# Optimization experiments

Measured on AMD Instinct MI355X. Metric: run time of the kernel, lower is better.

Reference implementation:

```python
import jax, jax.numpy as jnp
import numpy as np

NUM_CLASSES = 80
STRIDES = (32, 16, 8)
SCORE_THRESH = 0.01
NMS_THRESH = 0.45
TOP_K = 200
PRE_K = 4096          # pre-NMS candidate cap (greedy NMS only ever emits TOP_K boxes)
NEG = -1e9            # 'suppressed' score sentinel (avoids -inf NaN issues)
CLS_OFFSET = 4096.0   # class-aware NMS: offset boxes per class (boxes live in [0, 608])

_ANCHORS_PX = [[(116, 90), (156, 198), (373, 326)],
               [(30, 61), (62, 45), (59, 119)],
               [(10, 13), (16, 30), (33, 23)]]


def setup_inputs() -> dict:
    key = jax.random.key(0)
    bs, img = 8, 608
    inp = {}
    for lvl, (stride, anc) in enumerate(zip(STRIDES, _ANCHORS_PX)):
        H = W = img // stride
        key, k = jax.random.split(key)
        inp[f"in{lvl}"] = jax.random.normal(k, (bs, 3 * (NUM_CLASSES + 5), H, W), dtype=jnp.float32)
        aw = jnp.array([a[0] / stride for a in anc], jnp.float32)
        ah = jnp.array([a[1] / stride for a in anc], jnp.float32)
        inp[f"aw{lvl}"] = jnp.broadcast_to(aw[None, :, None, None], (bs, 3, H, W))
        inp[f"ah{lvl}"] = jnp.broadcast_to(ah[None, :, None, None], (bs, 3, H, W))
        inp[f"gx{lvl}"] = jnp.broadcast_to(jnp.arange(W, dtype=jnp.float32)[None, None, None, :], (bs, 3, H, W))
        inp[f"gy{lvl}"] = jnp.broadcast_to(jnp.arange(H, dtype=jnp.float32)[None, None, :, None], (bs, 3, H, W))
    return inp


def _decode_level(x, aw, ah, gx, gy, stride):
    bs, _, H, W = x.shape
    x = x.reshape(bs, -1, NUM_CLASSES + 5, H, W).transpose(0, 1, 3, 4, 2)  # [bs,3,H,W,85]
    px = jax.nn.sigmoid(x[..., 0]) + gx
    py = jax.nn.sigmoid(x[..., 1]) + gy
    pw = jnp.exp(x[..., 2]) * aw
    ph = jnp.exp(x[..., 3]) * ah
    conf = jax.nn.sigmoid(x[..., 4])
    cls = jax.nn.sigmoid(x[..., 5:])
    boxes = jnp.stack([px, py, pw, ph], -1) * jnp.float32(stride)  # [bs,3,H,W,4] (cx,cy,w,h)
    return boxes.reshape(bs, -1, 4), conf.reshape(bs, -1), cls.reshape(bs, -1, NUM_CLASSES)


def _center_to_corner(b):
    cx, cy, w, h = b[..., 0], b[..., 1], b[..., 2], b[..., 3]
    return jnp.stack([cx - w / 2, cy - h / 2, cx + w / 2, cy + h / 2], -1)


def _nms_image(boxes, conf, cls):
    # boxes [N,4] corner, conf [N], cls [N,C]
    N, C = cls.shape
    scores = (conf[:, None] * cls).reshape(-1)                          # [N*C]
    cboxes = jnp.broadcast_to(boxes[:, None, :], (N, C, 4)).reshape(-1, 4)
    labels = jnp.broadcast_to(jnp.arange(C), (N, C)).reshape(-1)
    s = jnp.where(scores > SCORE_THRESH, scores, NEG)
    top_s, idx = jax.lax.top_k(s, PRE_K)
    b = cboxes[idx]                                                     # [PRE_K,4]
    l = labels[idx]
    ob = b + (l.astype(jnp.float32) * CLS_OFFSET)[:, None]              # class-aware offset
    area = (ob[:, 2] - ob[:, 0]) * (ob[:, 3] - ob[:, 1])

    def step(live, _):
        i = jnp.argmax(live)
        si, bi, ai = live[i], ob[i], area[i]
        x1 = jnp.maximum(bi[0], ob[:, 0]); y1 = jnp.maximum(bi[1], ob[:, 1])
        x2 = jnp.minimum(bi[2], ob[:, 2]); y2 = jnp.minimum(bi[3], ob[:, 3])
        inter = jnp.clip(x2 - x1, 0.0) * jnp.clip(y2 - y1, 0.0)
        iou = inter / (ai + area - inter + 1e-9)
        live = jnp.where(iou > NMS_THRESH, NEG, live)                   # suppresses self too
        return live, (i, si)

    _, (sel, sel_s) = jax.lax.scan(step, top_s, None, length=TOP_K)
    valid = sel_s > SCORE_THRESH
    out_b = jnp.where(valid[:, None], b[sel], 0.0)
    out_l = jnp.where(valid, l[sel], 0).astype(jnp.float32)
    out_s = jnp.where(valid, sel_s, 0.0)
    return jnp.concatenate([out_b, out_l[:, None], out_s[:, None]], -1)  # [TOP_K, 6]


def _forward(levels):
    boxes, conf, cls = [], [], []
    for (x, aw, ah, gx, gy), stride in zip(levels, STRIDES):
        bb, cc, cl = _decode_level(x, aw, ah, gx, gy, stride)
        boxes.append(bb); conf.append(cc); cls.append(cl)
    boxes = _center_to_corner(jnp.concatenate(boxes, 1))   # [bs,N,4]
    conf = jnp.concatenate(conf, 1)                        # [bs,N]
    cls = jnp.concatenate(cls, 1)                          # [bs,N,C]
    return jax.vmap(_nms_image)(boxes, conf, cls)          # [bs,TOP_K,6]


def reference(in0, aw0, ah0, gx0, gy0, in1, aw1, ah1, gx1, gy1, in2, aw2, ah2, gx2, gy2):
    levels = [(in0, aw0, ah0, gx0, gy0), (in1, aw1, ah1, gx1, gy1), (in2, aw2, ah2, gx2, gy2)]
    return _forward(levels)
```

## Files before the change

kernel.cpp:

```cpp
#include <hip/hip_runtime.h>
#include <stdint.h>

typedef unsigned int u32;
typedef unsigned long long u64;

#define NCLS 80
#define NBOX 22743
#define PREK 4096
#define BCAP 65536
#define NIMG 8
#define SCORE_TH 0.01f
#define IOU_TH 0.45f
#define TOPK 200

#define DCH 20
#define DNCH 4
#define GCH 10
#define GNCH 8

#define LCAP 1536

#define BKCAP 8
#define HCAP 224
#define HUGE_TH 3488.0f

#define RJC 4
#define RJW 1024

#define HIST_OFF 0
#define META_OFF 131072
#define CNT_OFF  131200
#define ZERO_BYTES 133248
#define WIN_OFF  133248
#define BND_OFF  395392
#define PART_OFF BND_OFF
#define BOX_OFF  4589696
#define SKEY_OFF 7500800
#define SOBOX_OFF 7762944
#define SAREA_OFF 8287232

__device__ __forceinline__ float sigmf(float x) { return 1.0f / (1.0f + expf(-x)); }

#define BIN_BASE 61440u

__device__ __forceinline__ u64 pad_key(int i) { return (u64)(~(u32)i); }

__global__ __launch_bounds__(256) void decode_hist_all(const float* __restrict__ in0,
                              const float* __restrict__ in1, const float* __restrict__ in2,
                              float4* __restrict__ boxes, u32* __restrict__ hist) {
  __shared__ u32 lh[4096];
  const int img = blockIdx.y;
  const int c0 = blockIdx.z * DCH;
  for (int i = threadIdx.x; i < 4096; i += 256) lh[i] = 0;
  __syncthreads();

  const int bx = blockIdx.x;
  if (bx < 5) {
    const int W = 19, HW = 361;
    const int r = bx * 256 + threadIdx.x;
    if (r < 3 * HW) {
      const int a = r / HW, p = r - a * HW;
      const int y = p / W, x = p - y * W;
      const float* base = in0 + ((size_t)(img * 255 + a * 85)) * (size_t)HW + p;
      float l[DCH];
#pragma unroll
      for (int k = 0; k < DCH; ++k) l[k] = base[(size_t)(5 + c0 + k) * HW];
      const float x4 = base[4 * (size_t)HW];
      if (c0 == 0) {
        const float aw = (a == 0) ? 3.625f : ((a == 1) ? 4.875f : 11.65625f);
        const float ah = (a == 0) ? 2.8125f : ((a == 1) ? 6.1875f : 10.1875f);
        const float x0 = base[0];
        const float x1 = base[(size_t)HW];
        const float x2 = base[2 * (size_t)HW];
        const float x3 = base[3 * (size_t)HW];
        const float px = sigmf(x0) + (float)x;
        const float py = sigmf(x1) + (float)y;
        const float pw = expf(x2) * aw;
        const float ph = expf(x3) * ah;
        const float cx = px * 32.f, cy = py * 32.f, bw = pw * 32.f, bh = ph * 32.f;
        boxes[(size_t)img * NBOX + r] =
            make_float4(cx - bw * 0.5f, cy - bh * 0.5f, cx + bw * 0.5f, cy + bh * 0.5f);
      }
      const float conf = sigmf(x4);
      if (conf > SCORE_TH) {
#pragma unroll
        for (int k = 0; k < DCH; ++k) {
          float s = conf * sigmf(l[k]);
          if (s > SCORE_TH) {
            u32 bin = (__float_as_uint(s) >> 14) - BIN_BASE;
            atomicAdd(&lh[bin], 1u);
          }
        }
      }
    }
  } else {
    const bool L1 = bx < 10;
    const float* in = L1 ? in1 : in2;
    const int W = L1 ? 38 : 76;
    const int HW = L1 ? 1444 : 5776;
    const int lvl_off = L1 ? 1083 : 5415;
    const float stride = L1 ? 16.f : 8.f;
    const int HW4 = HW >> 2;
    const int idx = (bx - (L1 ? 5 : 10)) * 256 + threadIdx.x;
    if (idx < 3 * HW4) {
      const int a = idx / HW4;
      const int p0 = (idx - a * HW4) << 2;
      const float* base = in + ((size_t)(img * 255 + a * 85)) * (size_t)HW + p0;
      float4 scv[DCH];
#pragma unroll
      for (int k = 0; k < DCH; ++k)
        scv[k] = *(const float4*)(base + (size_t)(5 + c0 + k) * HW);
      float4 v4 = *(const float4*)(base + 4 * (size_t)HW);
      const float* t4 = (const float*)&v4;
      float conf[4];
      if (c0 == 0) {
        const float aw = L1 ? ((a == 0) ? 1.875f : ((a == 1) ? 3.875f : 3.6875f))
                            : ((a == 0) ? 1.25f : ((a == 1) ? 2.f : 4.125f));
        const float ah = L1 ? ((a == 0) ? 3.8125f : ((a == 1) ? 2.8125f : 7.4375f))
                            : ((a == 0) ? 1.625f : ((a == 1) ? 3.75f : 2.875f));
        float4 v0 = *(const float4*)(base);
        float4 v1 = *(const float4*)(base + (size_t)HW);
        float4 v2 = *(const float4*)(base + 2 * (size_t)HW);
        float4 v3 = *(const float4*)(base + 3 * (size_t)HW);
        const float* t0 = (const float*)&v0;
        const float* t1 = (const float*)&v1;
        const float* t2 = (const float*)&v2;
        const float* t3 = (const float*)&v3;
        float4* bout = boxes + (size_t)img * NBOX + lvl_off + a * HW + p0;
#pragma unroll
        for (int i = 0; i < 4; ++i) {
          const int p = p0 + i;
          const int y = p / W, x = p - y * W;
          const float px = sigmf(t0[i]) + (float)x;
          const float py = sigmf(t1[i]) + (float)y;
          const float pw = expf(t2[i]) * aw;
          const float ph = expf(t3[i]) * ah;
          const float cx = px * stride, cy = py * stride, bw = pw * stride, bh = ph * stride;
          bout[i] = make_float4(cx - bw * 0.5f, cy - bh * 0.5f, cx + bw * 0.5f, cy + bh * 0.5f);
        }
      }
#pragma unroll
      for (int i = 0; i < 4; ++i) conf[i] = sigmf(t4[i]);
#pragma unroll
      for (int k = 0; k < DCH; ++k) {
        const float* s4 = (const float*)&scv[k];
#pragma unroll
        for (int i = 0; i < 4; ++i) {
          float s = conf[i] * sigmf(s4[i]);
          if (s > SCORE_TH) {
            u32 bin = (__float_as_uint(s) >> 14) - BIN_BASE;
            atomicAdd(&lh[bin], 1u);
          }
        }
      }
    }
  }
  __syncthreads();
  u32* gh = hist + (size_t)img * 4096;
  for (int i = threadIdx.x; i < 4096; i += 256) {
    u32 v = lh[i];
    if (v) atomicAdd(&gh[i], v);
  }
}

__global__ void scan_k(const u32* __restrict__ hist, int* __restrict__ meta) {
  const int img = blockIdx.x;
  const u32* h = hist + (size_t)img * 4096;
  __shared__ u32 lsum[256];
  __shared__ u32 above[256];
  __shared__ u32 s_total;
  const int t = threadIdx.x;
  u32 s = 0;
  for (int j = 0; j < 16; ++j) s += h[t * 16 + j];
  lsum[t] = s;
  __syncthreads();
  if (t == 0) {
    u32 acc = 0;
    for (int i = 255; i >= 0; --i) { above[i] = acc; acc += lsum[i]; }
    s_total = acc;
  }
  __syncthreads();
  const u32 K = PREK;
  int* m = meta + img * 4;
  if (s_total < K) {
    if (t == 0) { m[0] = -1; m[1] = 0; }
  } else {
    if (above[t] < K && above[t] + lsum[t] >= K) {
      u32 cum = above[t];
      for (int j = 15; j >= 0; --j) {
        u32 hv = h[t * 16 + j];
        cum += hv;
        if (cum >= K) { m[0] = t * 16 + j; m[1] = (int)(K - (cum - hv)); break; }
      }
    }
  }
}

__device__ __forceinline__ void flush_list(const u64* llist, int lcnt, int cap,
                                           int* gctr, u64* glist, int gcap) {
  __shared__ int gbase_s;
  int n = lcnt < cap ? lcnt : cap;
  if (threadIdx.x == 0) gbase_s = n ? atomicAdd(gctr, n) : 0;
  __syncthreads();
  const int gb = gbase_s;
  for (int i = threadIdx.x; i < n; i += 256) {
    int pos = gb + i;
    if (pos < gcap) glist[pos] = llist[i];
  }
}

__global__ __launch_bounds__(256) void gather_all(const float* __restrict__ in0,
                         const float* __restrict__ in1, const float* __restrict__ in2,
                         const int* __restrict__ meta, int* __restrict__ cnt,
                         u64* __restrict__ winners, u64* __restrict__ boundary) {
  __shared__ u64 lwin[LCAP];
  __shared__ u64 lbnd[LCAP];
  __shared__ int lwc, lbc;
  const int img = blockIdx.y;
  const int c0 = blockIdx.z * GCH;
  if (threadIdx.x == 0) { lwc = 0; lbc = 0; }
  __syncthreads();

  const int B = meta[img * 4 + 0];
  int* cw = &cnt[img * 64];
  int* cb = &cnt[img * 64 + 32];
  u64* wl = winners + (size_t)img * PREK;
  u64* bl = boundary + (size_t)img * BCAP;
  const int bx = blockIdx.x;

  if (bx < 5) {
    const int HW = 361;
    const int r = bx * 256 + threadIdx.x;
    if (r < 3 * HW) {
      const int a = r / HW, p = r - a * HW;
      const float* base = in0 + ((size_t)(img * 255 + a * 85)) * (size_t)HW + p;
      const int boxg = r;
      float l[GCH];
#pragma unroll
      for (int k = 0; k < GCH; ++k) l[k] = base[(size_t)(5 + c0 + k) * HW];
      const float conf = sigmf(base[4 * (size_t)HW]);
#pragma unroll
      for (int k = 0; k < GCH; ++k) {
        float s = conf * sigmf(l[k]);
        if (s > SCORE_TH) {
          u32 key = __float_as_uint(s);
          int wbin = (int)((key >> 14) - BIN_BASE);
          if (wbin >= B) {
            u64 kv = ((u64)key << 32) | (u64)(~(u32)(boxg * NCLS + (c0 + k)));
            if (wbin > B) {
              int p2 = atomicAdd(&lwc, 1);
              if (p2 < LCAP) lwin[p2] = kv;
              else { int g = atomicAdd(cw, 1); if (g < PREK) wl[g] = kv; }
            } else {
              int p2 = atomicAdd(&lbc, 1);
              if (p2 < LCAP) lbnd[p2] = kv;
              else { int g = atomicAdd(cb, 1); if (g < BCAP) bl[g] = kv; }
            }
          }
        }
      }
    }
  } else {
    const bool L1 = bx < 10;
    const float* in = L1 ? in1 : in2;
    const int HW = L1 ? 1444 : 5776;
    const int lvl_off = L1 ? 1083 : 5415;
    const int HW4 = HW >> 2;
    const int idx = (bx - (L1 ? 5 : 10)) * 256 + threadIdx.x;
    if (idx < 3 * HW4) {
      const int a = idx / HW4;
      const int p0 = (idx - a * HW4) << 2;
      const float* base = in + ((size_t)(img * 255 + a * 85)) * (size_t)HW + p0;
      const int boxg0 = lvl_off + a * HW + p0;
      float4 scv[GCH];
#pragma unroll
      for (int k = 0; k < GCH; ++k)
        scv[k] = *(const float4*)(base + (size_t)(5 + c0 + k) * HW);
      float4 v4 = *(const float4*)(base + 4 * (size_t)HW);
      const float* t4 = (const float*)&v4;
      float conf[4];
#pragma unroll
      for (int i = 0; i < 4; ++i) conf[i] = sigmf(t4[i]);
#pragma unroll
      for (int k = 0; k < GCH; ++k) {
        const float* s4 = (const float*)&scv[k];
        const int c = c0 + k;
#pragma unroll
        for (int i = 0; i < 4; ++i) {
          float s = conf[i] * sigmf(s4[i]);
          if (s > SCORE_TH) {
            u32 key = __float_as_uint(s);
            int wbin = (int)((key >> 14) - BIN_BASE);
            if (wbin >= B) {
              u64 kv = ((u64)key << 32) | (u64)(~(u32)((boxg0 + i) * NCLS + c));
              if (wbin > B) {
                int p = atomicAdd(&lwc, 1);
                if (p < LCAP) lwin[p] = kv;
                else { int g = atomicAdd(cw, 1); if (g < PREK) wl[g] = kv; }
              } else {
                int p = atomicAdd(&lbc, 1);
                if (p < LCAP) lbnd[p] = kv;
                else { int g = atomicAdd(cb, 1); if (g < BCAP) bl[g] = kv; }
              }
            }
          }
        }
      }
    }
  }
  __syncthreads();
  flush_list(lwin, lwc, LCAP, cw, wl, PREK);
  flush_list(lbnd, lbc, LCAP, cb, bl, BCAP);
}

__global__ void resolve_k(const u64* __restrict__ boundary, const int* __restrict__ meta,
                          int* __restrict__ cnt, u64* __restrict__ winners) {
  const int img = blockIdx.x;
  const int T = meta[img * 4 + 1];
  int bc = cnt[img * 64 + 32];
  if (bc > BCAP) bc = BCAP;
  if (T <= 0 || bc <= 0) return;
  const u64* bnd = boundary + (size_t)img * BCAP;
  u64* wl = winners + (size_t)img * PREK;
  int* cw = &cnt[img * 64];

  __shared__ u32 h2[16384];
  __shared__ u32 lsum[256];
  __shared__ u32 above[256];
  __shared__ u32 s_total;
  __shared__ int sB2, sT2;
  __shared__ u64 ties[512];
  __shared__ int tcnt;
  __shared__ u64 lw2[PREK];
  __shared__ int lw2c;
  __shared__ int gbase_s;
  const int t = threadIdx.x;
  for (int i = t; i < 16384; i += 256) h2[i] = 0;
  if (t == 0) { tcnt = 0; sB2 = -1; sT2 = 0; lw2c = 0; }
  __syncthreads();
  for (int i = t; i < bc; i += 256) atomicAdd(&h2[(u32)(bnd[i] >> 32) & 0x3FFFu], 1u);
  __syncthreads();
  u32 s = 0;
  for (int j = 0; j < 64; ++j) s += h2[t * 64 + j];
  lsum[t] = s;
  __syncthreads();
  if (t == 0) {
    u32 acc = 0;
    for (int i = 255; i >= 0; --i) { above[i] = acc; acc += lsum[i]; }
    s_total = acc;
  }
  __syncthreads();
  if ((int)s_total > T) {
    if (above[t] < (u32)T && above[t] + lsum[t] >= (u32)T) {
      u32 cum = above[t];
      for (int j = 63; j >= 0; --j) {
        u32 hv = h2[t * 64 + j];
        cum += hv;
        if (cum >= (u32)T) { sB2 = t * 64 + j; sT2 = (int)((u32)T - (cum - hv)); break; }
      }
    }
  }
  __syncthreads();
  const int B2 = sB2, T2 = sT2;
  for (int i = t; i < bc; i += 256) {
    u64 e = bnd[i];
    int low = (int)((u32)(e >> 32) & 0x3FFFu);
    if (low > B2) {
      int p = atomicAdd(&lw2c, 1);
      if (p < PREK) lw2[p] = e;
    } else if (low == B2) {
      int tp = atomicAdd(&tcnt, 1);
      if (tp < 512) ties[tp] = e;
    }
  }
  __syncthreads();
  int n = lw2c < PREK ? lw2c : PREK;
  if (t == 0) gbase_s = n ? atomicAdd(cw, n) : 0;
  __syncthreads();
  for (int i = t; i < n; i += 256) {
    int pos = gbase_s + i;
    if (pos < PREK) wl[pos] = lw2[i];
  }
  __syncthreads();
  if (t == 0 && T2 > 0) {
    int tc = tcnt < 512 ? tcnt : 512;
    for (int k = 0; k < T2 && k < tc; ++k) {
      int bi = -1; u64 bk = 0;
      for (int i = 0; i < tc; ++i)
        if (ties[i] > bk) { bk = ties[i]; bi = i; }
      if (bi < 0) break;
      ties[bi] = 0;
      int pos = atomicAdd(cw, 1);
      if (pos < PREK) wl[pos] = bk;
    }
  }
}

__global__ __launch_bounds__(256) void rank_part_k(const u64* __restrict__ winners,
                                                   const int* __restrict__ cnt,
                                                   int* __restrict__ part) {
  __shared__ u64 lk[RJW];
  const int img = blockIdx.y;
  const int kc = blockIdx.x >> 2;
  const int jc = blockIdx.x & 3;
  const int t = threadIdx.x;
  int wc = cnt[img * 64]; if (wc > PREK) wc = PREK;
  const u64* wl = winners + (size_t)img * PREK;
  for (int i = t; i < RJW; i += 256) {
    const int gj = jc * RJW + i;
    lk[i] = (gj < wc) ? wl[gj] : pad_key(gj);
  }
  __syncthreads();
  const int ki_idx = kc * 256 + t;
  const u64 ki = (ki_idx < wc) ? wl[ki_idx] : pad_key(ki_idx);
  int rank = 0;
#pragma unroll 8
  for (int j = 0; j < RJW; ++j) rank += (lk[j] > ki) ? 1 : 0;
  part[(((size_t)img * RJC) + jc) * PREK + ki_idx] = rank;
}

__global__ __launch_bounds__(256) void rank_scatter_k(const u64* __restrict__ winners,
                                              const int* __restrict__ cnt,
                                              const int* __restrict__ part,
                                              const float4* __restrict__ boxes,
                                              u64* __restrict__ skey,
                                              float4* __restrict__ sobox,
                                              float* __restrict__ sarea) {
  const int img = blockIdx.y;
  const int i = blockIdx.x * 256 + threadIdx.x;
  int wc = cnt[img * 64]; if (wc > PREK) wc = PREK;
  const u64* wl = winners + (size_t)img * PREK;
  const u64 ki = (i < wc) ? wl[i] : pad_key(i);
  const int* pb = part + (size_t)img * RJC * PREK + i;
  int rank = pb[0] + pb[PREK] + pb[2 * PREK] + pb[3 * PREK];
  skey[(size_t)img * PREK + rank] = ki;
  if (i < wc) {
    u32 ridx = ~(u32)ki;
    int c = (int)(ridx % NCLS);
    int bi = (int)(ridx / NCLS);
    float4 b = boxes[(size_t)img * NBOX + bi];
    float off = 4096.0f * (float)c;
    float4 ob = make_float4(b.x + off, b.y + off, b.z + off, b.w + off);
    sobox[(size_t)img * PREK + rank] = ob;
    sarea[(size_t)img * PREK + rank] = (ob.z - ob.x) * (ob.w - ob.y);
  } else {
    sobox[(size_t)img * PREK + rank] = make_float4(0.f, 0.f, 0.f, 0.f);
    sarea[(size_t)img * PREK + rank] = 0.f;
  }
}

__global__ __launch_bounds__(64) void scan_nms_k(const u64* __restrict__ skey,
                                                 const float4* __restrict__ sobox,
                                                 const float* __restrict__ sarea,
                                                 float* __restrict__ out) {
  __shared__ float4 bxc[NCLS][BKCAP];
  __shared__ float  arc[NCLS][BKCAP];
  __shared__ int    cntc[NCLS];
  __shared__ float4 bxa[TOPK];
  __shared__ float  ara[TOPK];
  __shared__ float4 bxh[HCAP];
  __shared__ float  arh[HCAP];
  __shared__ int    nhuge_s;
  __shared__ float4 chb[64];
  __shared__ float  cha[64];
  const int img = blockIdx.x;
  const int lane = threadIdx.x;
  float* orow = out + (size_t)img * (TOPK * 6);
  for (int i = lane; i < TOPK * 6; i += 64) orow[i] = 0.f;
  for (int i = lane; i < NCLS; i += 64) cntc[i] = 0;
  if (lane == 0) nhuge_s = 0;
  const u64* K = skey + (size_t)img * PREK;
  const float4* Bp = sobox + (size_t)img * PREK;
  const float* Ap = sarea + (size_t)img * PREK;
  int nsel = 0;
  u64 kj = K[lane];
  float4 ob = Bp[lane];
  float ar = Ap[lane];
  for (int chunk = 0; chunk < PREK / 64 && nsel < TOPK; ++chunk) {
    u64 kj_n = 0ull; float4 ob_n = make_float4(0.f, 0.f, 0.f, 0.f); float ar_n = 0.f;
    if (chunk + 1 < PREK / 64) {
      const int jn = (chunk + 1) * 64 + lane;
      kj_n = K[jn]; ob_n = Bp[jn]; ar_n = Ap[jn];
    }
    const float score = __uint_as_float((u32)(kj >> 32));
    bool alive = (score > SCORE_TH);
    if (__ballot(alive) == 0ull) break;
    const u32 ridx = ~(u32)kj;
    const int myc = (int)(ridx % NCLS);
    const bool huge = (ob.z - ob.x > HUGE_TH) || (ob.w - ob.y > HUGE_TH);
    chb[lane] = ob; cha[lane] = ar;

    u64 mm = ~0ull;
#pragma unroll
    for (int k = 0; k < 7; ++k) {
      const u64 bk = __ballot(((myc >> k) & 1) != 0);
      mm &= (((myc >> k) & 1) != 0) ? bk : ~bk;
    }
    const u64 hb = __ballot(huge);

    {
      const int n0 = cntc[myc];
      const int n = n0 < BKCAP ? n0 : BKCAP;
      for (int k = 0; __ballot(alive && k < n) != 0ull; k += 2) {
        const int k0 = (k < BKCAP - 1) ? k : (BKCAP - 1);
        const int k1 = (k + 1 < BKCAP - 1) ? (k + 1) : (BKCAP - 1);
        const float4 b0 = bxc[myc][k0]; const float a0 = arc[myc][k0];
        const float4 b1 = bxc[myc][k1]; const float a1 = arc[myc][k1];
        if (alive && k < n) {
          float xx1 = fmaxf(b0.x, ob.x), yy1 = fmaxf(b0.y, ob.y);
          float xx2 = fminf(b0.z, ob.z), yy2 = fminf(b0.w, ob.w);
          float inter = fmaxf(xx2 - xx1, 0.f) * fmaxf(yy2 - yy1, 0.f);
          float iou = inter / (a0 + ar - inter + 1e-9f);
          if (iou > IOU_TH) alive = false;
        }
        if (alive && k + 1 < n) {
          float xx1 = fmaxf(b1.x, ob.x), yy1 = fmaxf(b1.y, ob.y);
          float xx2 = fminf(b1.z, ob.z), yy2 = fminf(b1.w, ob.w);
          float inter = fmaxf(xx2 - xx1, 0.f) * fmaxf(yy2 - yy1, 0.f);
          float iou = inter / (a1 + ar - inter + 1e-9f);
          if (iou > IOU_TH) alive = false;
        }
      }
    }
    {
      const int nh = nhuge_s;
      for (int k = 0; k < nh && __ballot(alive) != 0ull; k += 2) {
        const int k0 = (k < nh - 1) ? k : (nh - 1);
        const int k1 = (k + 1 < nh - 1) ? (k + 1) : (nh - 1);
        const float4 b0 = bxh[k0]; const float a0 = arh[k0];
        const float4 b1 = bxh[k1]; const float a1 = arh[k1];
        if (alive) {
          float xx1 = fmaxf(b0.x, ob.x), yy1 = fmaxf(b0.y, ob.y);
          float xx2 = fminf(b0.z, ob.z), yy2 = fminf(b0.w, ob.w);
          float inter = fmaxf(xx2 - xx1, 0.f) * fmaxf(yy2 - yy1, 0.f);
          float iou = inter / (a0 + ar - inter + 1e-9f);
          if (iou > IOU_TH) alive = false;
        }
        if (alive && k + 1 < nh) {
          float xx1 = fmaxf(b1.x, ob.x), yy1 = fmaxf(b1.y, ob.y);
          float xx2 = fminf(b1.z, ob.z), yy2 = fminf(b1.w, ob.w);
          float inter = fmaxf(xx2 - xx1, 0.f) * fmaxf(yy2 - yy1, 0.f);
          float iou = inter / (a1 + ar - inter + 1e-9f);
          if (iou > IOU_TH) alive = false;
        }
      }
    }
    if (__ballot(alive && huge) != 0ull) {
      const int na = nsel;
      for (int k = 0; k < na; k += 2) {
        const int k0 = (k < na - 1) ? k : (na - 1);
        const int k1 = (k + 1 < na - 1) ? (k + 1) : (na - 1);
        const float4 b0 = bxa[k0]; const float a0 = ara[k0];
        const float4 b1 = bxa[k1]; const float a1 = ara[k1];
        if (alive && huge) {
          float xx1 = fmaxf(b0.x, ob.x), yy1 = fmaxf(b0.y, ob.y);
          float xx2 = fminf(b0.z, ob.z), yy2 = fminf(b0.w, ob.w);
          float inter = fmaxf(xx2 - xx1, 0.f) * fmaxf(yy2 - yy1, 0.f);
          float iou = inter / (a0 + ar - inter + 1e-9f);
          if (iou > IOU_TH) alive = false;
        }
        if (alive && huge && k + 1 < na) {
          float xx1 = fmaxf(b1.x, ob.x), yy1 = fmaxf(b1.y, ob.y);
          float xx2 = fminf(b1.z, ob.z), yy2 = fminf(b1.w, ob.w);
          float inter = fmaxf(xx2 - xx1, 0.f) * fmaxf(yy2 - yy1, 0.f);
          float iou = inter / (a1 + ar - inter + 1e-9f);
          if (iou > IOU_TH) alive = false;
        }
        if (__ballot(alive && huge) == 0ull) break;
      }
    }
    const u64 amask = __ballot(alive);
    const u64 below = (1ull << lane) - 1ull;
    u64 tm = alive ? ((mm | hb | (huge ? ~0ull : 0ull)) & below & amask) : 0ull;
    u64 sup = 0ull;
    while (tm) {
      const int t = (int)__builtin_ctzll(tm);
      tm &= tm - 1ull;
      const float4 bj = chb[t];
      const float aj = cha[t];
      float xx1 = fmaxf(bj.x, ob.x), yy1 = fmaxf(bj.y, ob.y);
      float xx2 = fminf(bj.z, ob.z), yy2 = fminf(bj.w, ob.w);
      float inter = fmaxf(xx2 - xx1, 0.f) * fmaxf(yy2 - yy1, 0.f);
      float iou = inter / (aj + ar - inter + 1e-9f);
      if (iou > IOU_TH) sup |= (1ull << t);
    }
    u64 rem = amask;
    u64 selbits = 0ull;
    while (rem != 0ull && nsel + (int)__popcll(selbits) < TOPK) {
      const int b = __builtin_ctzll(rem);
      selbits |= (1ull << b);
      rem &= ~(1ull << b);
      const u64 colb = __ballot((sup >> b) & 1ull);
      rem &= ~colb;
    }
    const bool selme = (selbits >> lane) & 1ull;
    if (selme) {
      const int slot = nsel + (int)__popcll(selbits & ((1ull << lane) - 1ull));
      bxa[slot] = ob; ara[slot] = ar;
      if (!huge) {
        int cc = atomicAdd(&cntc[myc], 1);
        if (cc < BKCAP) { bxc[myc][cc] = ob; arc[myc][cc] = ar; }
        else { int hn = atomicAdd(&nhuge_s, 1); if (hn < HCAP) { bxh[hn] = ob; arh[hn] = ar; } }
      } else {
        int hn = atomicAdd(&nhuge_s, 1);
        if (hn < HCAP) { bxh[hn] = ob; arh[hn] = ar; }
      }
      const float off = 4096.0f * (float)myc;
      orow[slot * 6 + 0] = ob.x - off;
      orow[slot * 6 + 1] = ob.y - off;
      orow[slot * 6 + 2] = ob.z - off;
      orow[slot * 6 + 3] = ob.w - off;
      orow[slot * 6 + 4] = (float)myc;
      orow[slot * 6 + 5] = score;
    }
    nsel += (int)__popcll(selbits);
    kj = kj_n; ob = ob_n; ar = ar_n;
  }
}

extern "C" void kernel_launch(void* const* d_in, const int* in_sizes, int n_in,
                              void* d_out, int out_size, void* d_ws, size_t ws_size,
                              hipStream_t stream) {
  const float* in0 = (const float*)d_in[0];
  const float* in1 = (const float*)d_in[5];
  const float* in2 = (const float*)d_in[10];
  char* ws = (char*)d_ws;
  u32* hist = (u32*)(ws + HIST_OFF);
  int* meta = (int*)(ws + META_OFF);
  int* cnt = (int*)(ws + CNT_OFF);
  u64* winners = (u64*)(ws + WIN_OFF);
  u64* boundary = (u64*)(ws + BND_OFF);
  int* part = (int*)(ws + PART_OFF);
  float4* boxes = (float4*)(ws + BOX_OFF);
  u64* skey = (u64*)(ws + SKEY_OFF);
  float4* sobox = (float4*)(ws + SOBOX_OFF);
  float* sarea = (float*)(ws + SAREA_OFF);
  float* out = (float*)d_out;

  hipMemsetAsync(d_ws, 0, ZERO_BYTES, stream);

  decode_hist_all<<<dim3(27, 8, DNCH), 256, 0, stream>>>(in0, in1, in2, boxes, hist);

  scan_k<<<8, 256, 0, stream>>>(hist, meta);

  gather_all<<<dim3(27, 8, GNCH), 256, 0, stream>>>(in0, in1, in2, meta, cnt, winners, boundary);

  resolve_k<<<8, 256, 0, stream>>>(boundary, meta, cnt, winners);

  rank_part_k<<<dim3(64, 8), 256, 0, stream>>>(winners, cnt, part);
  rank_scatter_k<<<dim3(16, 8), 256, 0, stream>>>(winners, cnt, part, boxes, skey, sobox, sarea);
  scan_nms_k<<<8, 64, 0, stream>>>(skey, sobox, sarea, out);
}
```

Baseline: 117.1 us.

## Fuse histogram threshold scan into gather, replace memset, simplify NMS loops

Removes the separate scan_k launch by having every gather_all block redundantly compute the per-image threshold bin from the histogram using wave shuffles. resolve_k now derives the remaining boundary count from the winner counter instead of a stored meta value. The hipMemsetAsync is replaced by a small zeroing kernel, and the 2-way unrolled, ballot-guarded suppression loops in scan_nms_k become simple per-lane loops with early exit. This trades one kernel launch and a memset for redundant histogram reads in each gather block, and the NMS loop rewrite may change divergence behaviour.

Result: faster. 113.3 us (-3.2%).

```diff
diff --git a/kernel.cpp b/kernel.cpp
--- a/kernel.cpp
+++ b/kernel.cpp
@@ -28,7 +28,6 @@
 #define RJW 1024
 
 #define HIST_OFF 0
-#define META_OFF 131072
 #define CNT_OFF  131200
 #define ZERO_BYTES 133248
 #define WIN_OFF  133248
@@ -44,6 +43,11 @@
 #define BIN_BASE 61440u
 
 __device__ __forceinline__ u64 pad_key(int i) { return (u64)(~(u32)i); }
+
+__global__ __launch_bounds__(256) void init_k(uint4* __restrict__ ws) {
+  const int i = blockIdx.x * 256 + threadIdx.x;
+  if (i < ZERO_BYTES / 16) ws[i] = make_uint4(0u, 0u, 0u, 0u);
+}
 
 __global__ __launch_bounds__(256) void decode_hist_all(const float* __restrict__ in0,
                               const float* __restrict__ in1, const float* __restrict__ in2,
@@ -163,39 +167,6 @@
   }
 }
 
-__global__ void scan_k(const u32* __restrict__ hist, int* __restrict__ meta) {
-  const int img = blockIdx.x;
-  const u32* h = hist + (size_t)img * 4096;
-  __shared__ u32 lsum[256];
-  __shared__ u32 above[256];
-  __shared__ u32 s_total;
-  const int t = threadIdx.x;
-  u32 s = 0;
-  for (int j = 0; j < 16; ++j) s += h[t * 16 + j];
-  lsum[t] = s;
-  __syncthreads();
-  if (t == 0) {
-    u32 acc = 0;
-    for (int i = 255; i >= 0; --i) { above[i] = acc; acc += lsum[i]; }
-    s_total = acc;
-  }
-  __syncthreads();
-  const u32 K = PREK;
-  int* m = meta + img * 4;
-  if (s_total < K) {
-    if (t == 0) { m[0] = -1; m[1] = 0; }
-  } else {
-    if (above[t] < K && above[t] + lsum[t] >= K) {
-      u32 cum = above[t];
-      for (int j = 15; j >= 0; --j) {
-        u32 hv = h[t * 16 + j];
-        cum += hv;
-        if (cum >= K) { m[0] = t * 16 + j; m[1] = (int)(K - (cum - hv)); break; }
-      }
-    }
-  }
-}
-
 __device__ __forceinline__ void flush_list(const u64* llist, int lcnt, int cap,
                                            int* gctr, u64* glist, int gcap) {
   __shared__ int gbase_s;
@@ -211,17 +182,46 @@
 
 __global__ __launch_bounds__(256) void gather_all(const float* __restrict__ in0,
                          const float* __restrict__ in1, const float* __restrict__ in2,
-                         const int* __restrict__ meta, int* __restrict__ cnt,
+                         const u32* __restrict__ hist, int* __restrict__ cnt,
                          u64* __restrict__ winners, u64* __restrict__ boundary) {
   __shared__ u64 lwin[LCAP];
   __shared__ u64 lbnd[LCAP];
   __shared__ int lwc, lbc;
+  __shared__ u32 s_wsum[4];
+  __shared__ int sB;
   const int img = blockIdx.y;
   const int c0 = blockIdx.z * GCH;
-  if (threadIdx.x == 0) { lwc = 0; lbc = 0; }
-  __syncthreads();
-
-  const int B = meta[img * 4 + 0];
+  const int t = threadIdx.x;
+  if (t == 0) { lwc = 0; lbc = 0; sB = -1; }
+
+  {
+    const u32* gh = hist + (size_t)img * 4096;
+    u32 hv[16]; u32 s = 0;
+#pragma unroll
+    for (int j = 0; j < 16; ++j) { hv[j] = gh[t * 16 + j]; s += hv[j]; }
+    const int lane = t & 63;
+    u32 v = s;
+#pragma unroll
+    for (int off = 1; off < 64; off <<= 1) {
+      u32 o = __shfl_down(v, off);
+      if (lane + off < 64) v += o;
+    }
+    if (lane == 0) s_wsum[t >> 6] = v;
+    __syncthreads();
+    u32 hi = 0;
+    for (int w = (t >> 6) + 1; w < 4; ++w) hi += s_wsum[w];
+    const u32 above = hi + (v - s);
+    if (above < (u32)PREK && above + s >= (u32)PREK) {
+      u32 cum = above;
+      for (int j = 15; j >= 0; --j) {
+        cum += hv[j];
+        if (cum >= (u32)PREK) { sB = t * 16 + j; break; }
+      }
+    }
+    __syncthreads();
+  }
+  const int B = sB;
+
   int* cw = &cnt[img * 64];
   int* cb = &cnt[img * 64 + 32];
   u64* wl = winners + (size_t)img * PREK;
@@ -230,7 +230,7 @@
 
   if (bx < 5) {
     const int HW = 361;
-    const int r = bx * 256 + threadIdx.x;
+    const int r = bx * 256 + t;
     if (r < 3 * HW) {
       const int a = r / HW, p = r - a * HW;
       const float* base = in0 + ((size_t)(img * 255 + a * 85)) * (size_t)HW + p;
@@ -266,7 +266,7 @@
     const int HW = L1 ? 1444 : 5776;
     const int lvl_off = L1 ? 1083 : 5415;
     const int HW4 = HW >> 2;
-    const int idx = (bx - (L1 ? 5 : 10)) * 256 + threadIdx.x;
+    const int idx = (bx - (L1 ? 5 : 10)) * 256 + t;
     if (idx < 3 * HW4) {
       const int a = idx / HW4;
       const int p0 = (idx - a * HW4) << 2;
@@ -313,10 +313,11 @@
   flush_list(lbnd, lbc, LCAP, cb, bl, BCAP);
 }
 
-__global__ void resolve_k(const u64* __restrict__ boundary, const int* __restrict__ meta,
+__global__ void resolve_k(const u64* __restrict__ boundary,
                           int* __restrict__ cnt, u64* __restrict__ winners) {
   const int img = blockIdx.x;
-  const int T = meta[img * 4 + 1];
+  const int cw_pre = cnt[img * 64];
+  const int T = PREK - cw_pre;
   int bc = cnt[img * 64 + 32];
   if (bc > BCAP) bc = BCAP;
   if (T <= 0 || bc <= 0) return;
@@ -501,72 +502,39 @@
     {
       const int n0 = cntc[myc];
       const int n = n0 < BKCAP ? n0 : BKCAP;
-      for (int k = 0; __ballot(alive && k < n) != 0ull; k += 2) {
-        const int k0 = (k < BKCAP - 1) ? k : (BKCAP - 1);
-        const int k1 = (k + 1 < BKCAP - 1) ? (k + 1) : (BKCAP - 1);
-        const float4 b0 = bxc[myc][k0]; const float a0 = arc[myc][k0];
-        const float4 b1 = bxc[myc][k1]; const float a1 = arc[myc][k1];
-        if (alive && k < n) {
+      for (int k = 0; k < n && alive; ++k) {
+        const float4 b0 = bxc[myc][k]; const float a0 = arc[myc][k];
+        float xx1 = fmaxf(b0.x, ob.x), yy1 = fmaxf(b0.y, ob.y);
+        float xx2 = fminf(b0.z, ob.z), yy2 = fminf(b0.w, ob.w);
+        float inter = fmaxf(xx2 - xx1, 0.f) * fmaxf(yy2 - yy1, 0.f);
+        float iou = inter / (a0 + ar - inter + 1e-9f);
+        if (iou > IOU_TH) alive = false;
+      }
+    }
+    {
+      const int nh = nhuge_s;
+      for (int k = 0; k < nh; ++k) {
+        if (alive) {
+          const float4 b0 = bxh[k]; const float a0 = arh[k];
           float xx1 = fmaxf(b0.x, ob.x), yy1 = fmaxf(b0.y, ob.y);
           float xx2 = fminf(b0.z, ob.z), yy2 = fminf(b0.w, ob.w);
           float inter = fmaxf(xx2 - xx1, 0.f) * fmaxf(yy2 - yy1, 0.f);
           float iou = inter / (a0 + ar - inter + 1e-9f);
           if (iou > IOU_TH) alive = false;
         }
-        if (alive && k + 1 < n) {
-          float xx1 = fmaxf(b1.x, ob.x), yy1 = fmaxf(b1.y, ob.y);
-          float xx2 = fminf(b1.z, ob.z), yy2 = fminf(b1.w, ob.w);
-          float inter = fmaxf(xx2 - xx1, 0.f) * fmaxf(yy2 - yy1, 0.f);
-          float iou = inter / (a1 + ar - inter + 1e-9f);
-          if (iou > IOU_TH) alive = false;
-        }
-      }
-    }
-    {
-      const int nh = nhuge_s;
-      for (int k = 0; k < nh && __ballot(alive) != 0ull; k += 2) {
-        const int k0 = (k < nh - 1) ? k : (nh - 1);
-        const int k1 = (k + 1 < nh - 1) ? (k + 1) : (nh - 1);
-        const float4 b0 = bxh[k0]; const float a0 = arh[k0];
-        const float4 b1 = bxh[k1]; const float a1 = arh[k1];
-        if (alive) {
+      }
+    }
+    if (__ballot(alive && huge) != 0ull) {
+      const int na = nsel;
+      for (int k = 0; k < na; ++k) {
+        if (alive && huge) {
+          const float4 b0 = bxa[k]; const float a0 = ara[k];
           float xx1 = fmaxf(b0.x, ob.x), yy1 = fmaxf(b0.y, ob.y);
           float xx2 = fminf(b0.z, ob.z), yy2 = fminf(b0.w, ob.w);
           float inter = fmaxf(xx2 - xx1, 0.f) * fmaxf(yy2 - yy1, 0.f);
           float iou = inter / (a0 + ar - inter + 1e-9f);
           if (iou > IOU_TH) alive = false;
         }
-        if (alive && k + 1 < nh) {
-          float xx1 = fmaxf(b1.x, ob.x), yy1 = fmaxf(b1.y, ob.y);
-          float xx2 = fminf(b1.z, ob.z), yy2 = fminf(b1.w, ob.w);
-          float inter = fmaxf(xx2 - xx1, 0.f) * fmaxf(yy2 - yy1, 0.f);
-          float iou = inter / (a1 + ar - inter + 1e-9f);
-          if (iou > IOU_TH) alive = false;
-        }
-      }
-    }
-    if (__ballot(alive && huge) != 0ull) {
-      const int na = nsel;
-      for (int k = 0; k < na; k += 2) {
-        const int k0 = (k < na - 1) ? k : (na - 1);
-        const int k1 = (k + 1 < na - 1) ? (k + 1) : (na - 1);
-        const float4 b0 = bxa[k0]; const float a0 = ara[k0];
-        const float4 b1 = bxa[k1]; const float a1 = ara[k1];
-        if (alive && huge) {
-          float xx1 = fmaxf(b0.x, ob.x), yy1 = fmaxf(b0.y, ob.y);
-          float xx2 = fminf(b0.z, ob.z), yy2 = fminf(b0.w, ob.w);
-          float inter = fmaxf(xx2 - xx1, 0.f) * fmaxf(yy2 - yy1, 0.f);
-          float iou = inter / (a0 + ar - inter + 1e-9f);
-          if (iou > IOU_TH) alive = false;
-        }
-        if (alive && huge && k + 1 < na) {
-          float xx1 = fmaxf(b1.x, ob.x), yy1 = fmaxf(b1.y, ob.y);
-          float xx2 = fminf(b1.z, ob.z), yy2 = fminf(b1.w, ob.w);
-          float inter = fmaxf(xx2 - xx1, 0.f) * fmaxf(yy2 - yy1, 0.f);
-          float iou = inter / (a1 + ar - inter + 1e-9f);
-          if (iou > IOU_TH) alive = false;
-        }
-        if (__ballot(alive && huge) == 0ull) break;
       }
     }
     const u64 amask = __ballot(alive);
@@ -574,15 +542,15 @@
     u64 tm = alive ? ((mm | hb | (huge ? ~0ull : 0ull)) & below & amask) : 0ull;
     u64 sup = 0ull;
     while (tm) {
-      const int t = (int)__builtin_ctzll(tm);
+      const int tb = (int)__builtin_ctzll(tm);
       tm &= tm - 1ull;
-      const float4 bj = chb[t];
-      const float aj = cha[t];
+      const float4 bj = chb[tb];
+      const float aj = cha[tb];
       float xx1 = fmaxf(bj.x, ob.x), yy1 = fmaxf(bj.y, ob.y);
       float xx2 = fminf(bj.z, ob.z), yy2 = fminf(bj.w, ob.w);
       float inter = fmaxf(xx2 - xx1, 0.f) * fmaxf(yy2 - yy1, 0.f);
       float iou = inter / (aj + ar - inter + 1e-9f);
-      if (iou > IOU_TH) sup |= (1ull << t);
+      if (iou > IOU_TH) sup |= (1ull << tb);
     }
     u64 rem = amask;
     u64 selbits = 0ull;
@@ -626,7 +594,6 @@
   const float* in2 = (const float*)d_in[10];
   char* ws = (char*)d_ws;
   u32* hist = (u32*)(ws + HIST_OFF);
-  int* meta = (int*)(ws + META_OFF);
   int* cnt = (int*)(ws + CNT_OFF);
   u64* winners = (u64*)(ws + WIN_OFF);
   u64* boundary = (u64*)(ws + BND_OFF);
@@ -637,15 +604,13 @@
   float* sarea = (float*)(ws + SAREA_OFF);
   float* out = (float*)d_out;
 
-  hipMemsetAsync(d_ws, 0, ZERO_BYTES, stream);
+  init_k<<<(ZERO_BYTES / 16 + 255) / 256, 256, 0, stream>>>((uint4*)ws);
 
   decode_hist_all<<<dim3(27, 8, DNCH), 256, 0, stream>>>(in0, in1, in2, boxes, hist);
 
-  scan_k<<<8, 256, 0, stream>>>(hist, meta);
-
-  gather_all<<<dim3(27, 8, GNCH), 256, 0, stream>>>(in0, in1, in2, meta, cnt, winners, boundary);
-
-  resolve_k<<<8, 256, 0, stream>>>(boundary, meta, cnt, winners);
+  gather_all<<<dim3(27, 8, GNCH), 256, 0, stream>>>(in0, in1, in2, hist, cnt, winners, boundary);
+
+  resolve_k<<<8, 256, 0, stream>>>(boundary, cnt, winners);
 
   rank_part_k<<<dim3(64, 8), 256, 0, stream>>>(winners, cnt, part);
   rank_scatter_k<<<dim3(16, 8), 256, 0, stream>>>(winners, cnt, part, boxes, skey, sobox, sarea);
```
